# Performance work log

Hardware: AMD Instinct MI355X
Metric: run time of the kernel (lower is better)

Reference implementation:

```python
import jax, jax.numpy as jnp
import numpy as np

# Model dims
P_SPECS = [(6, 256), (7, 256)]          # pattern_length -> num_patterns (ordered)
P = 512                                  # total_num_patterns
MAXL = 7                                 # max_pattern_length
ND = 2                                   # num_diags (self-loop diag + main diag)
D = 300                                  # embedding_dim
V = 50000                                # vocab size
B = 32                                   # batch size
T = 128                                  # max_doc_len
NC = 2                                   # num_classes
NEG = -1e30                              # max-sum semiring zero; one = 0.0
END_STATES = np.concatenate([np.full(n, l - 1, dtype=np.int32) for l, n in P_SPECS])


def setup_inputs() -> dict:
    key = jax.random.key(0)
    ks = jax.random.split(key, 8)
    tokens = jax.random.randint(ks[0], (B, T), 0, V, dtype=jnp.int32)
    doc_lens = jax.random.randint(ks[1], (B,), 64, T + 1, dtype=jnp.int32)
    emb_table = jax.random.normal(ks[2], (V, D), dtype=jnp.float32)
    diags = jax.random.normal(ks[3], (P * ND * MAXL, D), dtype=jnp.float32)
    diags = diags / jnp.linalg.norm(diags, axis=1, keepdims=True)  # normalize(diags)
    bias = jax.random.normal(ks[4], (P * ND * MAXL, 1), dtype=jnp.float32)
    epsilons = jax.random.normal(ks[5], (P, MAXL - 1), dtype=jnp.float32)
    bn_weight = jnp.ones((P,), jnp.float32)
    bn_bias = jnp.zeros((P,), jnp.float32)
    final_w = 0.05 * jax.random.normal(ks[6], (NC, P), dtype=jnp.float32)
    final_b = jnp.zeros((NC,), jnp.float32)
    return dict(tokens=tokens, doc_lens=doc_lens, emb_table=emb_table, diags=diags,
                bias=bias, epsilons=epsilons, bn_weight=bn_weight, bn_bias=bn_bias,
                final_w=final_w, final_b=final_b)


def reference(tokens, doc_lens, emb_table, diags, bias, epsilons,
              bn_weight, bn_bias, final_w, final_b):
    # --- transition matrices (max-sum semiring: from_outer is identity) ---
    emb = emb_table[tokens]                                   # [B,T,D]
    # mm(diags, embeddings) + bias_scale * bias  (bias_scale = 1.0)
    ts = jnp.einsum('btd,kd->btk', emb, diags) + bias[:, 0]   # [B,T,P*ND*MAXL]
    ts = ts.reshape(B, T, P, ND, MAXL)                        # [B,T,P,ND,MAXL]

    end = jnp.asarray(END_STATES)                             # [P]
    hid0 = jnp.full((B, P, MAXL), NEG, jnp.float32).at[:, :, 0].set(0.0)
    sc0 = jnp.full((B, P), NEG, jnp.float32)                  # semiring.zero
    zpad = jnp.full((B, P, 1), NEG, jnp.float32)              # zero_padding
    rpad = jnp.zeros((B, P, 1), jnp.float32)                  # restart_padding (one)

    # epsilon_values = epsilon_scale (one=0) + epsilons
    def step(carry, xs):
        hid, sc = carry
        tm, i = xs                                            # tm: [B,P,ND,MAXL]
        # epsilon transitions
        ae = jnp.maximum(hid, jnp.concatenate([zpad, hid[:, :, :-1] + epsilons], axis=2))
        # main path: diag index -1 (the main diagonal)
        main = jnp.concatenate([rpad, ae[:, :, :-1] + tm[:, :, -1, :-1]], axis=2)
        # self loops: diag 0, self_loop_scale = semiring.one = 0
        sl = ae + tm[:, :, 0, :]
        hid = jnp.maximum(main, sl)
        endv = jnp.take_along_axis(hid, jnp.broadcast_to(end[None, :, None], (B, P, 1)), axis=2)[:, :, 0]
        sc = jnp.where((doc_lens > i)[:, None], jnp.maximum(sc, endv), sc)
        return (hid, sc), None

    (_, scores), _ = jax.lax.scan(step, (hid0, sc0),
                                  (jnp.moveaxis(ts, 1, 0), jnp.arange(T, dtype=jnp.int32)))

    # BatchNorm1d (training mode: biased batch statistics)
    mean = scores.mean(axis=0)
    var = scores.var(axis=0)
    scores = (scores - mean) * jax.lax.rsqrt(var + 1e-5) * bn_weight + bn_bias
    # binarize_scores
    scores = jnp.sign(jax.nn.relu(scores))
    # final linear layer
    return scores @ final_w.T + final_b                       # [B, NC]
```

## Files before the change

### kernel.cpp

```cpp
#include <hip/hip_runtime.h>

#define BB 32
#define TT 128
#define PP 512
#define DD 300
#define KT 10
#define AT 256
#define BT 448
#define CTS 114
#define NEG -1e30f

typedef _Float16 half8 __attribute__((ext_vector_type(8)));
typedef float floatx4 __attribute__((ext_vector_type(4)));

__device__ __forceinline__ void async_load16(const void* g, void* l) {
    __builtin_amdgcn_global_load_lds(
        (const __attribute__((address_space(1))) void*)g,
        (__attribute__((address_space(3))) void*)l, 16, 0, 0);
}

__device__ __forceinline__ floatx4 mfma16(half8 a, half8 b, floatx4 c) {
    return __builtin_amdgcn_mfma_f32_16x16x32_f16(a, b, c, 0, 0, 0);
}

__global__ __launch_bounds__(256) void pack_kernel(
    const int* __restrict__ tokens, const float* __restrict__ emb,
    const float* __restrict__ diags, const float* __restrict__ bias,
    _Float16* __restrict__ AhP, _Float16* __restrict__ AlP,
    _Float16* __restrict__ BhP, _Float16* __restrict__ BlP)
{
    const int idx = blockIdx.x * 256 + threadIdx.x;
    if (idx >= (AT + BT) * KT * 64) return;
    const int chunk = idx >> 6;
    const int ln = idx & 63;

    const float* src;
    float kslot;
    _Float16 *dh, *dl;
    int kt;
    if (chunk < AT * KT) {
        const int mt = chunk / KT; kt = chunk - mt * KT;
        const int m = mt * 16 + (ln & 15);
        src = emb + (size_t)tokens[m] * DD;
        kslot = 1.0f;
        dh = AhP + (size_t)chunk * 512 + ln * 8;
        dl = AlP + (size_t)chunk * 512 + ln * 8;
    } else {
        const int c2 = chunk - AT * KT;
        const int nt = c2 / KT; kt = c2 - nt * KT;
        const int n = nt * 16 + (ln & 15);
        src = diags + (size_t)n * DD;
        kslot = bias[n];
        dh = BhP + (size_t)c2 * 512 + ln * 8;
        dl = BlP + (size_t)c2 * 512 + ln * 8;
    }

    const int k0 = kt * 32 + (ln >> 4) * 8;
    float v[8];
    if (k0 + 8 <= DD) {
        float4 a = *(const float4*)(src + k0);
        float4 b = *(const float4*)(src + k0 + 4);
        v[0] = a.x; v[1] = a.y; v[2] = a.z; v[3] = a.w;
        v[4] = b.x; v[5] = b.y; v[6] = b.z; v[7] = b.w;
    } else {
        #pragma unroll
        for (int i = 0; i < 8; ++i) {
            const int k = k0 + i;
            v[i] = (k < DD) ? src[k] : (k == DD ? kslot : 0.f);
        }
    }
    half8 h, l;
    #pragma unroll
    for (int i = 0; i < 8; ++i) {
        h[i] = (_Float16)v[i];
        l[i] = (_Float16)((v[i] - (float)h[i]) * 4096.f);
    }
    *(half8*)dh = h;
    *(half8*)dl = l;
}

__global__ __launch_bounds__(256, 2) void gemm_scan_kernel(
    const _Float16* __restrict__ AhP, const _Float16* __restrict__ AlP,
    const _Float16* __restrict__ BhP, const _Float16* __restrict__ BlP,
    const float* __restrict__ epsilons,
    const int* __restrict__ doc_lens,
    float* __restrict__ scores)
{
    __shared__ __align__(16) unsigned char smem[128 * CTS * 4];
    typedef _Float16 BsT[2][7][512];
    BsT* Bs = reinterpret_cast<BsT*>(smem);
    float (*Ct)[CTS] = reinterpret_cast<float(*)[CTS]>(smem);

    const int tid = threadIdx.x;
    const int w = tid >> 6, ln = tid & 63;
    const int bx = blockIdx.x;
    const int b  = blockIdx.y;

    floatx4 acc0[2][7], acc1[2][7];
    #pragma unroll
    for (int i = 0; i < 2; ++i)
        #pragma unroll
        for (int j = 0; j < 7; ++j) {
            acc0[i][j] = (floatx4){0.f, 0.f, 0.f, 0.f};
            acc1[i][j] = (floatx4){0.f, 0.f, 0.f, 0.f};
        }

    half8 ah[2][2], al[2][2];

    auto loadA = [&](int kt, int pb) {
        #pragma unroll
        for (int i = 0; i < 2; ++i) {
            const size_t ch = ((size_t)(b * 8 + 2 * w + i) * KT + kt) * 512 + ln * 8;
            ah[pb][i] = *(const half8*)(AhP + ch);
            al[pb][i] = *(const half8*)(AlP + ch);
        }
    };
    auto stageB = [&](int kt, int buf) {
        #pragma unroll
        for (int s = 0; s < 4; ++s) {
            const int cidx = w + 4 * s;
            if (cidx < 14) {
                const int nt = cidx >> 1, hl = cidx & 1;
                const size_t ch = ((size_t)(7 * bx + nt) * KT + kt) * 512 + ln * 8;
                async_load16((hl ? BlP : BhP) + ch, &Bs[buf][hl][nt][0]);
            }
        }
    };

    stageB(0, 0);
    loadA(0, 0);
    __syncthreads();

    #pragma unroll
    for (int kt = 0; kt < KT; ++kt) {
        const int cb = kt & 1, nb = cb ^ 1;
        if (kt + 1 < KT) {
            loadA(kt + 1, nb);
            stageB(kt + 1, nb);
        }
        #pragma unroll
        for (int j = 0; j < 7; ++j) {
            const half8 bh = *(const half8*)&Bs[cb][0][j][ln * 8];
            const half8 bl = *(const half8*)&Bs[cb][1][j][ln * 8];
            #pragma unroll
            for (int i = 0; i < 2; ++i) {
                acc0[i][j] = mfma16(ah[cb][i], bh, acc0[i][j]);
                acc1[i][j] = mfma16(ah[cb][i], bl, acc1[i][j]);
                acc1[i][j] = mfma16(al[cb][i], bh, acc1[i][j]);
            }
        }
        __syncthreads();
    }

    #pragma unroll
    for (int j = 0; j < 7; ++j) {
        const int col = j * 16 + (ln & 15);
        #pragma unroll
        for (int i = 0; i < 2; ++i) {
            const int rb = (2 * w + i) * 16 + (ln >> 4) * 4;
            #pragma unroll
            for (int r = 0; r < 4; ++r)
                Ct[rb + r][col] = acc0[i][j][r] + acc1[i][j][r] * (1.0f / 4096.0f);
        }
    }
    __syncthreads();
    if (w != 0) return;
    if (ln >= 8) return;

    const int p = bx * 8 + ln;
    const int dl = doc_lens[b];
    const int c0 = ln * 14;
    const bool end5 = (p < 256);

    float e[6];
    #pragma unroll
    for (int i = 0; i < 6; ++i) e[i] = epsilons[p * 6 + i];

    float h0 = 0.f, h1 = NEG, h2 = NEG, h3 = NEG, h4 = NEG, h5 = NEG, h6 = NEG;
    float sc = NEG;

    float2 fa[7], fb[7];
    auto ldrow = [&](int t, float2* f) {
        const float* row = &Ct[t][c0];
        #pragma unroll
        for (int i = 0; i < 7; ++i) f[i] = *(const float2*)(row + 2 * i);
    };
    auto stepv = [&](const float2* v) {
        float ae0 = h0;
        float ae1 = fmaxf(h1, h0 + e[0]);
        float ae2 = fmaxf(h2, h1 + e[1]);
        float ae3 = fmaxf(h3, h2 + e[2]);
        float ae4 = fmaxf(h4, h3 + e[3]);
        float ae5 = fmaxf(h5, h4 + e[4]);
        float ae6 = fmaxf(h6, h5 + e[5]);
        h0 = fmaxf(0.f,          ae0 + v[0].x);
        h1 = fmaxf(ae0 + v[3].y, ae1 + v[0].y);
        h2 = fmaxf(ae1 + v[4].x, ae2 + v[1].x);
        h3 = fmaxf(ae2 + v[4].y, ae3 + v[1].y);
        h4 = fmaxf(ae3 + v[5].x, ae4 + v[2].x);
        h5 = fmaxf(ae4 + v[5].y, ae5 + v[2].y);
        h6 = fmaxf(ae5 + v[6].x, ae6 + v[3].x);
        sc = fmaxf(sc, end5 ? h5 : h6);
    };

    ldrow(0, fa);
    int t = 0;
    for (; t + 2 <= dl; t += 2) {
        ldrow(t + 1, fb);
        stepv(fa);
        ldrow(t + 2 <= 127 ? t + 2 : 127, fa);
        stepv(fb);
    }
    if (t < dl) stepv(fa);

    scores[p * BB + b] = sc;
}

__global__ __launch_bounds__(512) void finalize_kernel(
    const float* __restrict__ scores,
    const float* __restrict__ bn_w,
    const float* __restrict__ bn_b,
    const float* __restrict__ fw,
    const float* __restrict__ fb,
    float* __restrict__ out)
{
    __shared__ float acc[64];
    const int p = threadIdx.x;
    if (p < 64) acc[p] = 0.f;
    __syncthreads();

    float x[32];
    const float4* sp = (const float4*)(scores + p * 32);
    #pragma unroll
    for (int i = 0; i < 8; ++i) ((float4*)x)[i] = sp[i];

    float mean = 0.f;
    #pragma unroll
    for (int i = 0; i < 32; ++i) mean += x[i];
    mean *= (1.f / 32.f);
    float var = 0.f;
    #pragma unroll
    for (int i = 0; i < 32; ++i) { const float d = x[i] - mean; var = fmaf(d, d, var); }
    var *= (1.f / 32.f);

    const float scale = (1.f / sqrtf(var + 1e-5f)) * bn_w[p];
    const float shift = bn_b[p];
    const float w0 = fw[p], w1 = fw[PP + p];

    for (int b = 0; b < 32; ++b) {
        const float v = (x[b] - mean) * scale + shift;
        const bool bin = v > 0.f;
        float v0 = bin ? w0 : 0.f;
        float v1 = bin ? w1 : 0.f;
        #pragma unroll
        for (int o = 32; o; o >>= 1) {
            v0 += __shfl_xor(v0, o);
            v1 += __shfl_xor(v1, o);
        }
        if ((threadIdx.x & 63) == 0) {
            atomicAdd(&acc[b * 2 + 0], v0);
            atomicAdd(&acc[b * 2 + 1], v1);
        }
    }
    __syncthreads();
    if (p < 64) out[p] = acc[p] + fb[p & 1];
}

extern "C" void kernel_launch(void* const* d_in, const int* in_sizes, int n_in,
                              void* d_out, int out_size, void* d_ws, size_t ws_size,
                              hipStream_t stream) {
    const int*   tokens   = (const int*)d_in[0];
    const int*   doc_lens = (const int*)d_in[1];
    const float* emb      = (const float*)d_in[2];
    const float* diags    = (const float*)d_in[3];
    const float* bias     = (const float*)d_in[4];
    const float* eps      = (const float*)d_in[5];
    const float* bnw      = (const float*)d_in[6];
    const float* bnb      = (const float*)d_in[7];
    const float* fw       = (const float*)d_in[8];
    const float* fb       = (const float*)d_in[9];
    float* out = (float*)d_out;

    float* scores = (float*)d_ws;
    _Float16* AhP = (_Float16*)(scores + PP * BB);
    _Float16* AlP = AhP + (size_t)AT * KT * 512;
    _Float16* BhP = AlP + (size_t)AT * KT * 512;
    _Float16* BlP = BhP + (size_t)BT * KT * 512;

    pack_kernel<<<(AT + BT) * KT * 64 / 256, 256, 0, stream>>>(
        tokens, emb, diags, bias, AhP, AlP, BhP, BlP);
    gemm_scan_kernel<<<dim3(64, BB), 256, 0, stream>>>(
        AhP, AlP, BhP, BlP, eps, doc_lens, scores);
    finalize_kernel<<<1, 512, 0, stream>>>(scores, bnw, bnb, fw, fb, out);
}
```

Measured before the change: 216.2 us.

## Skip GEMM for padded time rows and deepen scan prefetch with raised priority

Each wave whose 32-row time slice lies entirely past the document length now skips its A loads and MFMA work. It still participates in B staging and the barriers, so the block stays in sync. The serial scan now keeps a four-deep ring of prefetched LDS rows instead of two, and raises wave priority during the scan to hide LDS latency on the critical sequential path. Rows past doc_len are left uninitialized in the Ct tile, but they are never read by the scan.

```diff
diff --git a/kernel.cpp b/kernel.cpp
--- a/kernel.cpp
+++ b/kernel.cpp
@@ -96,6 +96,9 @@
     const int bx = blockIdx.x;
     const int b  = blockIdx.y;
 
+    const int dl = doc_lens[b];
+    const bool live = (32 * w < dl);
+
     floatx4 acc0[2][7], acc1[2][7];
     #pragma unroll
     for (int i = 0; i < 2; ++i)
@@ -128,39 +131,50 @@
     };
 
     stageB(0, 0);
-    loadA(0, 0);
+    if (live) loadA(0, 0);
     __syncthreads();
 
-    #pragma unroll
-    for (int kt = 0; kt < KT; ++kt) {
-        const int cb = kt & 1, nb = cb ^ 1;
-        if (kt + 1 < KT) {
-            loadA(kt + 1, nb);
-            stageB(kt + 1, nb);
-        }
+    if (live) {
+        #pragma unroll
+        for (int kt = 0; kt < KT; ++kt) {
+            const int cb = kt & 1, nb = cb ^ 1;
+            if (kt + 1 < KT) {
+                loadA(kt + 1, nb);
+                stageB(kt + 1, nb);
+            }
+            #pragma unroll
+            for (int j = 0; j < 7; ++j) {
+                const half8 bh = *(const half8*)&Bs[cb][0][j][ln * 8];
+                const half8 bl = *(const half8*)&Bs[cb][1][j][ln * 8];
+                #pragma unroll
+                for (int i = 0; i < 2; ++i) {
+                    acc0[i][j] = mfma16(ah[cb][i], bh, acc0[i][j]);
+                    acc1[i][j] = mfma16(ah[cb][i], bl, acc1[i][j]);
+                    acc1[i][j] = mfma16(al[cb][i], bh, acc1[i][j]);
+                }
+            }
+            __syncthreads();
+        }
+    } else {
+        #pragma unroll
+        for (int kt = 0; kt < KT; ++kt) {
+            const int nb = (kt & 1) ^ 1;
+            if (kt + 1 < KT) stageB(kt + 1, nb);
+            __syncthreads();
+        }
+    }
+
+    if (live) {
         #pragma unroll
         for (int j = 0; j < 7; ++j) {
-            const half8 bh = *(const half8*)&Bs[cb][0][j][ln * 8];
-            const half8 bl = *(const half8*)&Bs[cb][1][j][ln * 8];
+            const int col = j * 16 + (ln & 15);
             #pragma unroll
             for (int i = 0; i < 2; ++i) {
-                acc0[i][j] = mfma16(ah[cb][i], bh, acc0[i][j]);
-                acc1[i][j] = mfma16(ah[cb][i], bl, acc1[i][j]);
-                acc1[i][j] = mfma16(al[cb][i], bh, acc1[i][j]);
+                const int rb = (2 * w + i) * 16 + (ln >> 4) * 4;
+                #pragma unroll
+                for (int r = 0; r < 4; ++r)
+                    Ct[rb + r][col] = acc0[i][j][r] + acc1[i][j][r] * (1.0f / 4096.0f);
             }
-        }
-        __syncthreads();
-    }
-
-    #pragma unroll
-    for (int j = 0; j < 7; ++j) {
-        const int col = j * 16 + (ln & 15);
-        #pragma unroll
-        for (int i = 0; i < 2; ++i) {
-            const int rb = (2 * w + i) * 16 + (ln >> 4) * 4;
-            #pragma unroll
-            for (int r = 0; r < 4; ++r)
-                Ct[rb + r][col] = acc0[i][j][r] + acc1[i][j][r] * (1.0f / 4096.0f);
         }
     }
     __syncthreads();
@@ -168,7 +182,6 @@
     if (ln >= 8) return;
 
     const int p = bx * 8 + ln;
-    const int dl = doc_lens[b];
     const int c0 = ln * 14;
     const bool end5 = (p < 256);
 
@@ -179,13 +192,14 @@
     float h0 = 0.f, h1 = NEG, h2 = NEG, h3 = NEG, h4 = NEG, h5 = NEG, h6 = NEG;
     float sc = NEG;
 
-    float2 fa[7], fb[7];
-    auto ldrow = [&](int t, float2* f) {
+    float2 buf[4][7];
+    auto load = [&](int slot, int t) {
         const float* row = &Ct[t][c0];
         #pragma unroll
-        for (int i = 0; i < 7; ++i) f[i] = *(const float2*)(row + 2 * i);
+        for (int i = 0; i < 7; ++i) buf[slot][i] = *(const float2*)(row + 2 * i);
     };
-    auto stepv = [&](const float2* v) {
+    auto step = [&](int slot) {
+        const float2* v = buf[slot];
         float ae0 = h0;
         float ae1 = fmaxf(h1, h0 + e[0]);
         float ae2 = fmaxf(h2, h1 + e[1]);
@@ -203,15 +217,24 @@
         sc = fmaxf(sc, end5 ? h5 : h6);
     };
 
-    ldrow(0, fa);
-    int t = 0;
-    for (; t + 2 <= dl; t += 2) {
-        ldrow(t + 1, fb);
-        stepv(fa);
-        ldrow(t + 2 <= 127 ? t + 2 : 127, fa);
-        stepv(fb);
-    }
-    if (t < dl) stepv(fa);
+    __builtin_amdgcn_s_setprio(1);
+    #pragma unroll
+    for (int j = 0; j < 4; ++j) load(j, j);
+
+    int tb = 0;
+    for (; tb + 4 <= dl; tb += 4) {
+        #pragma unroll
+        for (int j = 0; j < 4; ++j) {
+            step(j);
+            const int t = tb + j + 4;
+            load(j, t > 127 ? 127 : t);
+        }
+    }
+    const int rem = dl - tb;
+    #pragma unroll
+    for (int j = 0; j < 3; ++j)
+        if (j < rem) step(j);
+    __builtin_amdgcn_s_setprio(0);
 
     scores[p * BB + b] = sc;
 }
```

Measured after the change: 230.4 us. 6.6% more time.
